# Kernel optimization log

Hardware: AMD Instinct MI355X
Metric: run time of the kernel (lower is better)

## Reference

```python
import math
import jax, jax.numpy as jnp
import numpy as np

B, S, D = 2, 2048, 512
H = 8
DH = D // H  # 64
FF = 2048


def _uniform(key, shape, c):
    return jax.random.uniform(key, shape, jnp.float32, -c, c)


def setup_inputs() -> dict:
    key = jax.random.key(0)
    ks = jax.random.split(key, 16)
    x = jax.random.normal(ks[0], (B, S, D), jnp.float32)
    c_qkv = math.sqrt(6 / (D + DH))
    wq = _uniform(ks[1], (H, D, DH), c_qkv)
    wk = _uniform(ks[2], (H, D, DH), c_qkv)
    wv = _uniform(ks[3], (H, D, DH), c_qkv)
    bq = jnp.zeros((H, DH), jnp.float32)
    bk = jnp.zeros((H, DH), jnp.float32)
    bv = jnp.zeros((H, DH), jnp.float32)
    c_o = math.sqrt(6 / (H * DH + D))
    wo = _uniform(ks[4], (H * DH, D), c_o)  # stored as (in, out)
    bo = jnp.zeros((D,), jnp.float32)
    gamma1 = jnp.ones((D,), jnp.float32)
    beta1 = jnp.zeros((D,), jnp.float32)
    c_ff = math.sqrt(6 / (D + FF))
    w1 = _uniform(ks[5], (D, FF), c_ff)
    b1 = jnp.zeros((FF,), jnp.float32)
    w2 = _uniform(ks[6], (FF, D), c_ff)
    b2 = jnp.zeros((D,), jnp.float32)
    gamma2 = jnp.ones((D,), jnp.float32)
    beta2 = jnp.zeros((D,), jnp.float32)
    return dict(x=x, wq=wq, bq=bq, wk=wk, bk=bk, wv=wv, bv=bv, wo=wo, bo=bo,
                gamma1=gamma1, beta1=beta1, w1=w1, b1=b1, w2=w2, b2=b2,
                gamma2=gamma2, beta2=beta2)


def _layernorm(x, gamma, beta):
    # matches torch: (x - mean) / std(unbiased=False), no epsilon in denom
    mean = jnp.mean(x, axis=-1, keepdims=True)
    var = jnp.mean((x - mean) ** 2, axis=-1, keepdims=True)
    return gamma * (x - mean) / jnp.sqrt(var) + beta


def reference(x, wq, bq, wk, bk, wv, bv, wo, bo, gamma1, beta1, w1, b1, w2, b2, gamma2, beta2):
    # multi-head attention: all heads batched in one einsum (same math as the per-head loop)
    q = jnp.einsum('bsd,hde->bhse', x, wq) + bq[None, :, None, :]
    k = jnp.einsum('bsd,hde->bhse', x, wk) + bk[None, :, None, :]
    v = jnp.einsum('bsd,hde->bhse', x, wv) + bv[None, :, None, :]
    scores = jnp.einsum('bhse,bhte->bhst', q, k) / math.sqrt(DH)  # [B,H,S,S]
    attn = jax.nn.softmax(scores, axis=-1)
    y = jnp.einsum('bhst,bhte->bhse', attn, v)  # [B,H,S,DH]
    y = y.transpose(0, 2, 1, 3).reshape(B, S, H * DH)
    y = y @ wo + bo
    # residual + LN (dropout is identity in eval)
    y = _layernorm(y + x, gamma1, beta1)
    # feedforward
    f = jax.nn.relu(y @ w1 + b1) @ w2 + b2
    out = _layernorm(f + y, gamma2, beta2)
    return out
```

## Files before the change

kernel.cpp:

```cpp
#include <hip/hip_runtime.h>

typedef __bf16 bf16;
typedef __attribute__((ext_vector_type(8))) __bf16 bf16x8;
typedef __attribute__((ext_vector_type(4))) float f32x4;
typedef __attribute__((ext_vector_type(16))) float f32x16;

#define DEV __device__ __forceinline__

DEV f32x4 mfma16(bf16x8 a, bf16x8 b, f32x4 c) {
  return __builtin_amdgcn_mfma_f32_16x16x32_bf16(a, b, c, 0, 0, 0);
}
DEV f32x16 mfma32(bf16x8 a, bf16x8 b, f32x16 c) {
  return __builtin_amdgcn_mfma_f32_32x32x16_bf16(a, b, c, 0, 0, 0);
}
DEV void gll16(const bf16* g, bf16* l) {
  __builtin_amdgcn_global_load_lds(
      (const __attribute__((address_space(1))) void*)g,
      (__attribute__((address_space(3))) void*)l, 16, 0, 0);
}
DEV unsigned cvtpk(float a, float b) {
  unsigned r;
  asm("v_cvt_pk_bf16_f32 %0, %1, %2" : "=v"(r) : "v"(a), "v"(b));
  return r;
}
DEV void pl32swap(unsigned& x, unsigned& y) {
  asm("v_permlane32_swap_b32 %0, %1" : "+v"(x), "+v"(y));
}

__global__ __launch_bounds__(256) void prep_k(
    const float* __restrict__ x, const float* __restrict__ wq,
    const float* __restrict__ wk, const float* __restrict__ wv,
    const float* __restrict__ wo, const float* __restrict__ w1,
    const float* __restrict__ w2, const float* __restrict__ bq,
    const float* __restrict__ bk, const float* __restrict__ bv,
    bf16* __restrict__ xb, bf16* __restrict__ wqkvT, bf16* __restrict__ woT,
    bf16* __restrict__ w1T, bf16* __restrict__ w2T, float* __restrict__ cb) {
  const int blk = blockIdx.x, tid = threadIdx.x;
  if (blk < 1024) {
    int i = blk * 256 + tid;
    const float4* p = (const float4*)x + (size_t)i * 2;
    float4 a = p[0], b = p[1];
    bf16x8 o;
    o[0] = (bf16)a.x; o[1] = (bf16)a.y; o[2] = (bf16)a.z; o[3] = (bf16)a.w;
    o[4] = (bf16)b.x; o[5] = (bf16)b.y; o[6] = (bf16)b.z; o[7] = (bf16)b.w;
    ((bf16x8*)xb)[i] = o;
    return;
  }
  if (blk == 1792) {
    for (int i = tid; i < 1536; i += 256)
      cb[i] = i < 512 ? bq[i] : (i < 1024 ? bk[i - 512] : bv[i - 1024]);
    return;
  }
  __shared__ float tile[64][65];
  const int t = blk - 1024;
  const float* src;
  bf16* dst;
  int C, Rout, r0, c0;
  if (t < 192) {
    int mat = t / 64, rem = t % 64, head = rem >> 3, rt = rem & 7;
    src = (mat == 0 ? wq : mat == 1 ? wk : wv) + head * 32768;
    dst = wqkvT + (size_t)(mat * 8 + head) * 32768;
    C = 64; Rout = 512; r0 = rt * 64; c0 = 0;
  } else if (t < 256) {
    int t2 = t - 192;
    src = wo; dst = woT; C = 512; Rout = 512;
    r0 = (t2 >> 3) * 64; c0 = (t2 & 7) * 64;
  } else if (t < 512) {
    int t2 = t - 256;
    src = w1; dst = w1T; C = 2048; Rout = 512;
    r0 = (t2 >> 5) * 64; c0 = (t2 & 31) * 64;
  } else {
    int t2 = t - 512;
    src = w2; dst = w2T; C = 512; Rout = 2048;
    r0 = (t2 >> 3) * 64; c0 = (t2 & 7) * 64;
  }
#pragma unroll
  for (int j = 0; j < 4; ++j) {
    int e = j * 256 + tid;
    int r = e >> 4, c4 = e & 15;
    float4 f = *(const float4*)(src + (size_t)(r0 + r) * C + c0 + c4 * 4);
    tile[r][c4 * 4 + 0] = f.x;
    tile[r][c4 * 4 + 1] = f.y;
    tile[r][c4 * 4 + 2] = f.z;
    tile[r][c4 * 4 + 3] = f.w;
  }
  __syncthreads();
  const int co = tid >> 2, rr0 = (tid & 3) * 16;
  bf16x8 o0, o1;
#pragma unroll
  for (int k = 0; k < 8; ++k) o0[k] = (bf16)tile[rr0 + k][co];
#pragma unroll
  for (int k = 0; k < 8; ++k) o1[k] = (bf16)tile[rr0 + 8 + k][co];
  bf16* dp = dst + (size_t)(c0 + co) * Rout + r0 + rr0;
  *(bf16x8*)dp = o0;
  *(bf16x8*)(dp + 8) = o1;
}

__global__ __launch_bounds__(256) void vtrans_k(const bf16* __restrict__ qkv,
                                                bf16* __restrict__ vtb) {
  __shared__ bf16 tile[64 * 68];
  const int tid = threadIdx.x;
  const int s0 = blockIdx.x * 64;
  const int bh = blockIdx.y, b = bh >> 3, hh = bh & 7;
  const bf16* src = qkv + 1024 + hh * 64;
#pragma unroll
  for (int j = 0; j < 2; ++j) {
    int slot = j * 256 + tid;
    int r = slot >> 3, cc = slot & 7;
    *(bf16x8*)(tile + r * 68 + cc * 8) =
        *(const bf16x8*)(src + (size_t)(b * 2048 + s0 + r) * 1536 + cc * 8);
  }
  __syncthreads();
  const int w = tid >> 6, lane = tid & 63;
#pragma unroll
  for (int sb2 = 0; sb2 < 2; ++sb2) {
    int sb = w * 2 + sb2;
    bf16x8 v;
#pragma unroll
    for (int jj = 0; jj < 8; ++jj) v[jj] = tile[(sb * 8 + jj) * 68 + lane];
    *(bf16x8*)(vtb + (size_t)bh * 131072 + (size_t)lane * 2048 + s0 + sb * 8) = v;
  }
}

template <int EPI>
__global__ __launch_bounds__(256) void gemmN64(
    const bf16* __restrict__ A, const bf16* __restrict__ Bt,
    const float* __restrict__ bias, float* __restrict__ outf,
    bf16* __restrict__ outb, int M, int N, int K, int klen) {
  __shared__ bf16 As[128 * 64];
  __shared__ bf16 Bs[64 * 64];
  const int tid = threadIdx.x;
  const int w = tid >> 6, l = tid & 63;
  const int lh = l & 15, lg = l >> 4;
  const int m0 = blockIdx.x * 128, n0 = blockIdx.y * 64;
  const int k0 = blockIdx.z * klen;
  const int mb = (w & 1) * 64, nb = (w >> 1) * 32;
  f32x4 acc[4][2] = {};
  for (int kt = k0; kt < k0 + klen; kt += 64) {
    __syncthreads();
#pragma unroll
    for (int j = 0; j < 4; ++j) {
      int slot = j * 256 + tid;
      int r = slot >> 3, cc = slot & 7;
      int kk = kt + ((cc ^ (r & 7)) << 3);
      gll16(A + (size_t)(m0 + r) * K + kk, As + slot * 8);
    }
#pragma unroll
    for (int j = 0; j < 2; ++j) {
      int slot = j * 256 + tid;
      int r = slot >> 3, cc = slot & 7;
      int kk = kt + ((cc ^ (r & 7)) << 3);
      gll16(Bt + (size_t)(n0 + r) * K + kk, Bs + slot * 8);
    }
    __syncthreads();
#pragma unroll
    for (int kk = 0; kk < 2; ++kk) {
      bf16x8 af[4], bfr[2];
#pragma unroll
      for (int mi = 0; mi < 4; ++mi) {
        int r = mb + mi * 16 + lh;
        af[mi] = *(const bf16x8*)(As + r * 64 + (((kk * 4 + lg) ^ (r & 7)) << 3));
      }
#pragma unroll
      for (int ni = 0; ni < 2; ++ni) {
        int r = nb + ni * 16 + lh;
        bfr[ni] = *(const bf16x8*)(Bs + r * 64 + (((kk * 4 + lg) ^ (r & 7)) << 3));
      }
#pragma unroll
      for (int mi = 0; mi < 4; ++mi)
#pragma unroll
        for (int ni = 0; ni < 2; ++ni)
          acc[mi][ni] = mfma16(af[mi], bfr[ni], acc[mi][ni]);
    }
  }
  float* op = (EPI == 0) ? outf + (size_t)blockIdx.z * M * N : nullptr;
#pragma unroll
  for (int mi = 0; mi < 4; ++mi)
#pragma unroll
    for (int ni = 0; ni < 2; ++ni)
#pragma unroll
      for (int i = 0; i < 4; ++i) {
        int row = m0 + mb + mi * 16 + lg * 4 + i;
        int col = n0 + nb + ni * 16 + lh;
        float v = acc[mi][ni][i];
        if (EPI == 0) {
          op[(size_t)row * N + col] = v;
        } else if (EPI == 1) {
          v += bias[col];
          outb[(size_t)row * N + col] = (bf16)fmaxf(v, 0.f);
        } else {
          v += bias[col];
          outb[(size_t)row * N + col] = (bf16)(col < 512 ? v * 0.125f : v);
        }
      }
}

__global__ __launch_bounds__(256) void attn_fwd5(
    const bf16* __restrict__ qkv,
    const bf16* __restrict__ vtb,
    bf16* __restrict__ Y) {
  __shared__ __align__(16) char lds[65536];
  const int tid = threadIdx.x;
  const int w = tid >> 6, lane = tid & 63;
  const int l31 = lane & 31, h = lane >> 5;
  const int bh = blockIdx.y, b = bh >> 3, hh = bh & 7;
  const int qt = blockIdx.x;
  const int wp = w & 1, half = w >> 1;
  const int q0 = qt * 64 + wp * 32;

  bf16x8 qf[4];
  {
    const size_t rowQ = (size_t)(b * 2048 + q0 + l31) * 1536 + hh * 64;
#pragma unroll
    for (int g = 0; g < 4; ++g)
      qf[g] = *(const bf16x8*)(qkv + rowQ + g * 16 + h * 8);
  }
  const bf16* Kp = qkv + 512 + hh * 64;
  const bf16* Vp = vtb + (size_t)bh * 131072;

  f32x16 oacc[2] = {};
  float m_run = -1e30f, l_run = 0.f;

#define KBUF(d, hf) ((bf16*)(lds + (d) * 32768 + (hf) * 16384))
#define VBUF(d, hf) ((bf16*)(lds + (d) * 32768 + (hf) * 16384 + 8192))

  auto stage = [&](int i, int d) {
#pragma unroll
    for (int hf = 0; hf < 2; ++hf) {
      const int k0 = hf * 1024 + i * 64;
#pragma unroll
      for (int j = 0; j < 2; ++j) {
        int slot = j * 256 + tid;
        int r = slot >> 3, cc = slot & 7;
        gll16(Kp + (size_t)(b * 2048 + k0 + r) * 1536 + ((cc ^ (r & 7)) << 3),
              KBUF(d, hf) + slot * 8);
        gll16(Vp + (size_t)r * 2048 + k0 + ((cc ^ (r & 7)) << 3),
              VBUF(d, hf) + slot * 8);
      }
    }
  };

  stage(0, 0);
  __syncthreads();
  for (int i = 0; i < 16; ++i) {
    const int d = i & 1;
    if (i < 15) stage(i + 1, d ^ 1);
    const bf16* Kt = KBUF(d, half);
    const bf16* Vt = VBUF(d, half);
    f32x16 st[2];
    __builtin_amdgcn_s_setprio(1);
#pragma unroll
    for (int kt = 0; kt < 2; ++kt) {
      f32x16 z = {};
      const int r = kt * 32 + l31;
#pragma unroll
      for (int g = 0; g < 4; ++g) {
        bf16x8 kf = *(const bf16x8*)(Kt + r * 64 + (((2 * g + h) ^ (r & 7)) << 3));
        z = mfma32(kf, qf[g], z);
      }
      st[kt] = z;
    }
    __builtin_amdgcn_s_setprio(0);
    float mx = -1e30f;
#pragma unroll
    for (int kt = 0; kt < 2; ++kt)
#pragma unroll
      for (int r = 0; r < 16; ++r) mx = fmaxf(mx, st[kt][r]);
    mx = fmaxf(mx, __shfl_xor(mx, 32, 64));
    const float m_new = fmaxf(m_run, mx);
    const float scl = __expf(m_run - m_new);
    m_run = m_new;
    float ps = 0.f;
#pragma unroll
    for (int kt = 0; kt < 2; ++kt)
#pragma unroll
      for (int r = 0; r < 16; ++r) {
        float e = __expf(st[kt][r] - m_new);
        st[kt][r] = e;
        ps += e;
      }
    ps += __shfl_xor(ps, 32, 64);
    l_run = l_run * scl + ps;
    oacc[0] = oacc[0] * scl;
    oacc[1] = oacc[1] * scl;
    bf16x8 pf[4];
#pragma unroll
    for (int kt = 0; kt < 2; ++kt)
#pragma unroll
      for (int g = 0; g < 2; ++g) {
        unsigned a0 = cvtpk(st[kt][8 * g + 0], st[kt][8 * g + 1]);
        unsigned a1 = cvtpk(st[kt][8 * g + 2], st[kt][8 * g + 3]);
        unsigned b0 = cvtpk(st[kt][8 * g + 4], st[kt][8 * g + 5]);
        unsigned b1 = cvtpk(st[kt][8 * g + 6], st[kt][8 * g + 7]);
        pl32swap(a0, b0);
        pl32swap(a1, b1);
        union { unsigned u[4]; bf16x8 v; } pk;
        pk.u[0] = a0; pk.u[1] = a1; pk.u[2] = b0; pk.u[3] = b1;
        pf[kt * 2 + g] = pk.v;
      }
    __builtin_amdgcn_s_setprio(1);
#pragma unroll
    for (int t = 0; t < 2; ++t) {
      const int r = t * 32 + l31;
#pragma unroll
      for (int kg = 0; kg < 4; ++kg) {
        bf16x8 vf = *(const bf16x8*)(Vt + r * 64 + (((2 * kg + h) ^ (r & 7)) << 3));
        oacc[t] = mfma32(vf, pf[kg], oacc[t]);
      }
    }
    __builtin_amdgcn_s_setprio(0);
    __syncthreads();
  }

  if (half == 1) {
    char* ob = lds + wp * 8192;
#pragma unroll
    for (int t = 0; t < 2; ++t)
#pragma unroll
      for (int c = 0; c < 4; ++c) {
        f32x4 v4 = {oacc[t][c * 4 + 0], oacc[t][c * 4 + 1],
                    oacc[t][c * 4 + 2], oacc[t][c * 4 + 3]};
        *(f32x4*)(ob + (t * 4 + c) * 1024 + lane * 16) = v4;
      }
    ((float2*)(lds + 32768))[wp * 64 + lane] = make_float2(m_run, l_run);
  }
  __syncthreads();
  bf16* Yt = (bf16*)(lds + 34816);
  if (half == 0) {
    float2 ml2 = ((const float2*)(lds + 32768))[wp * 64 + lane];
    const float mstar = fmaxf(m_run, ml2.x);
    const float e1 = __expf(m_run - mstar), e2 = __expf(ml2.x - mstar);
    const float lstar = l_run * e1 + ml2.y * e2;
    const float r1 = e1 / lstar, r2 = e2 / lstar;
    const char* ob = lds + wp * 8192;
#pragma unroll
    for (int t = 0; t < 2; ++t)
#pragma unroll
      for (int c = 0; c < 4; ++c) {
        f32x4 v4 = *(const f32x4*)(ob + (t * 4 + c) * 1024 + lane * 16);
#pragma unroll
        for (int j = 0; j < 4; ++j)
          oacc[t][c * 4 + j] = oacc[t][c * 4 + j] * r1 + v4[j] * r2;
      }
#pragma unroll
    for (int t = 0; t < 2; ++t)
#pragma unroll
      for (int r = 0; r < 16; ++r) {
        int dh = (r & 3) + 8 * (r >> 2) + 4 * h + 32 * t;
        Yt[(wp * 32 + l31) * 72 + dh] = (bf16)oacc[t][r];
      }
  }
  __syncthreads();
#pragma unroll
  for (int it = 0; it < 2; ++it) {
    int s = it * 256 + tid;
    int ql = s >> 3, cbk = s & 7;
    bf16x8 v = *(const bf16x8*)(Yt + ql * 72 + cbk * 8);
    *(bf16x8*)(Y + (size_t)(b * 2048 + qt * 64 + ql) * 512 + hh * 64 + cbk * 8) = v;
  }
#undef KBUF
#undef VBUF
}

__global__ __launch_bounds__(256) void add_ln1_k(
    const float* __restrict__ P,
    const float* __restrict__ xres, const float* __restrict__ bias,
    const float* __restrict__ gamma, const float* __restrict__ beta,
    bf16* __restrict__ outb) {
  const int row = blockIdx.x, tid = threadIdx.x;
  const size_t base = (size_t)row * 512;
  const float2 p0 = ((const float2*)(P + base))[tid];
  const float2 p1 = ((const float2*)(P + 2097152 + base))[tid];
  const float2 xr = ((const float2*)(xres + base))[tid];
  const int c = tid * 2;
  float s0 = p0.x + p1.x + bias[c] + xr.x;
  float s1 = p0.y + p1.y + bias[c + 1] + xr.y;
  float sum = s0 + s1;
#pragma unroll
  for (int m = 1; m < 64; m <<= 1) sum += __shfl_xor(sum, m, 64);
  __shared__ float part[4], part2[4];
  const int w = tid >> 6, l = tid & 63;
  if (l == 0) part[w] = sum;
  __syncthreads();
  const float mean = (part[0] + part[1] + part[2] + part[3]) * (1.f / 512.f);
  const float d0 = s0 - mean, d1 = s1 - mean;
  float vs = d0 * d0 + d1 * d1;
#pragma unroll
  for (int m = 1; m < 64; m <<= 1) vs += __shfl_xor(vs, m, 64);
  if (l == 0) part2[w] = vs;
  __syncthreads();
  const float var = (part2[0] + part2[1] + part2[2] + part2[3]) * (1.f / 512.f);
  const float inv = rsqrtf(var);
  outb[base + c] = (bf16)(gamma[c] * (d0 * inv) + beta[c]);
  outb[base + c + 1] = (bf16)(gamma[c + 1] * (d1 * inv) + beta[c + 1]);
}

__global__ __launch_bounds__(256) void add_ln2_k(
    const float* __restrict__ P,
    const bf16* __restrict__ rres, const float* __restrict__ bias,
    const float* __restrict__ gamma, const float* __restrict__ beta,
    float* __restrict__ outf) {
  const int row = blockIdx.x, tid = threadIdx.x;
  const size_t base = (size_t)row * 512;
  const float2 p0 = ((const float2*)(P + base))[tid];
  const float2 p1 = ((const float2*)(P + 2097152 + base))[tid];
  const int c = tid * 2;
  float s0 = p0.x + p1.x + bias[c] + (float)rres[base + c];
  float s1 = p0.y + p1.y + bias[c + 1] + (float)rres[base + c + 1];
  float sum = s0 + s1;
#pragma unroll
  for (int m = 1; m < 64; m <<= 1) sum += __shfl_xor(sum, m, 64);
  __shared__ float part[4], part2[4];
  const int w = tid >> 6, l = tid & 63;
  if (l == 0) part[w] = sum;
  __syncthreads();
  const float mean = (part[0] + part[1] + part[2] + part[3]) * (1.f / 512.f);
  const float d0 = s0 - mean, d1 = s1 - mean;
  float vs = d0 * d0 + d1 * d1;
#pragma unroll
  for (int m = 1; m < 64; m <<= 1) vs += __shfl_xor(vs, m, 64);
  if (l == 0) part2[w] = vs;
  __syncthreads();
  const float var = (part2[0] + part2[1] + part2[2] + part2[3]) * (1.f / 512.f);
  const float inv = rsqrtf(var);
  ((float2*)(outf + base))[tid] =
      make_float2(gamma[c] * (d0 * inv) + beta[c], gamma[c + 1] * (d1 * inv) + beta[c + 1]);
}

extern "C" void kernel_launch(void* const* d_in, const int* in_sizes, int n_in,
                              void* d_out, int out_size, void* d_ws, size_t ws_size,
                              hipStream_t stream) {
  const float* x = (const float*)d_in[0];
  const float* wq = (const float*)d_in[1];
  const float* bq = (const float*)d_in[2];
  const float* wk = (const float*)d_in[3];
  const float* bk = (const float*)d_in[4];
  const float* wv = (const float*)d_in[5];
  const float* bv = (const float*)d_in[6];
  const float* wo = (const float*)d_in[7];
  const float* bo = (const float*)d_in[8];
  const float* g1 = (const float*)d_in[9];
  const float* be1 = (const float*)d_in[10];
  const float* w1 = (const float*)d_in[11];
  const float* b1 = (const float*)d_in[12];
  const float* w2 = (const float*)d_in[13];
  const float* b2 = (const float*)d_in[14];
  const float* g2 = (const float*)d_in[15];
  const float* be2 = (const float*)d_in[16];

  char* ws = (char*)d_ws;
  bf16* xb    = (bf16*)(ws + 0);
  bf16* y1b   = (bf16*)(ws + 0);
  bf16* wqkvT = (bf16*)(ws + 4194304);
  bf16* woT   = (bf16*)(ws + 5767168);
  bf16* w1T   = (bf16*)(ws + 6291456);
  bf16* w2T   = (bf16*)(ws + 8388608);
  float* cb   = (float*)(ws + 10485760);
  bf16* qkvb  = (bf16*)(ws + 10493952);
  float* t0   = (float*)(ws + 10493952);
  bf16* f1    = (bf16*)(ws + 10493952);
  bf16* vtb   = (bf16*)(ws + 23078656);
  bf16* yb    = (bf16*)(ws + 27272960);
  float* f2   = (float*)(ws + 27272960);

  prep_k<<<1793, 256, 0, stream>>>(x, wq, wk, wv, wo, w1, w2, bq, bk, bv,
                                   xb, wqkvT, woT, w1T, w2T, cb);

  gemmN64<2><<<dim3(32, 24, 1), 256, 0, stream>>>(xb, wqkvT, cb, nullptr, qkvb,
                                                  4096, 1536, 512, 512);
  vtrans_k<<<dim3(32, 16), 256, 0, stream>>>(qkvb, vtb);
  attn_fwd5<<<dim3(32, 16), 256, 0, stream>>>(qkvb, vtb, yb);
  gemmN64<0><<<dim3(32, 8, 2), 256, 0, stream>>>(yb, woT, nullptr, t0, nullptr,
                                                 4096, 512, 512, 256);
  add_ln1_k<<<4096, 256, 0, stream>>>(t0, x, bo, g1, be1, y1b);
  gemmN64<1><<<dim3(32, 32, 1), 256, 0, stream>>>(y1b, w1T, b1, nullptr, f1,
                                                  4096, 2048, 512, 512);
  gemmN64<0><<<dim3(32, 8, 2), 256, 0, stream>>>(f1, w2T, nullptr, f2, nullptr,
                                                 4096, 512, 2048, 1024);
  add_ln2_k<<<4096, 256, 0, stream>>>(f2, y1b, b2, g2, be2, (float*)d_out);
}
```

Baseline: 119.9 us.

## Split attention KV range across four wave pairs with 512-thread blocks

The attention kernel now runs 8 waves per block instead of 4, splitting the 2048-key range into four quarters instead of two. Each iteration loads one tile per quarter, and four partial softmax states are merged at the end. Double buffering is dropped for a single-buffer load-then-sync loop. The row max and row sum reductions become tree reductions to shorten dependency chains. The aim is more waves to hide latency and more MFMA parallelism, at the cost of unoverlapped loads, an extra sync per iteration and a larger merge step.

```diff
diff --git a/kernel.cpp b/kernel.cpp
--- a/kernel.cpp
+++ b/kernel.cpp
@@ -195,7 +195,7 @@
       }
 }
 
-__global__ __launch_bounds__(256) void attn_fwd5(
+__global__ __launch_bounds__(512) void attn_fwd6(
     const bf16* __restrict__ qkv,
     const bf16* __restrict__ vtb,
     bf16* __restrict__ Y) {
@@ -205,7 +205,7 @@
   const int l31 = lane & 31, h = lane >> 5;
   const int bh = blockIdx.y, b = bh >> 3, hh = bh & 7;
   const int qt = blockIdx.x;
-  const int wp = w & 1, half = w >> 1;
+  const int wp = w & 1, hx = w >> 1;
   const int q0 = qt * 64 + wp * 32;
 
   bf16x8 qf[4];
@@ -221,32 +221,26 @@
   f32x16 oacc[2] = {};
   float m_run = -1e30f, l_run = 0.f;
 
-#define KBUF(d, hf) ((bf16*)(lds + (d) * 32768 + (hf) * 16384))
-#define VBUF(d, hf) ((bf16*)(lds + (d) * 32768 + (hf) * 16384 + 8192))
-
-  auto stage = [&](int i, int d) {
-#pragma unroll
-    for (int hf = 0; hf < 2; ++hf) {
-      const int k0 = hf * 1024 + i * 64;
-#pragma unroll
-      for (int j = 0; j < 2; ++j) {
-        int slot = j * 256 + tid;
-        int r = slot >> 3, cc = slot & 7;
-        gll16(Kp + (size_t)(b * 2048 + k0 + r) * 1536 + ((cc ^ (r & 7)) << 3),
-              KBUF(d, hf) + slot * 8);
-        gll16(Vp + (size_t)r * 2048 + k0 + ((cc ^ (r & 7)) << 3),
-              VBUF(d, hf) + slot * 8);
-      }
+#define KB6(q4) ((bf16*)(lds + (q4) * 16384))
+#define VB6(q4) ((bf16*)(lds + (q4) * 16384 + 8192))
+
+  auto stage = [&](int it) {
+    const int r = tid >> 3, cc = tid & 7;
+#pragma unroll
+    for (int q4 = 0; q4 < 4; ++q4) {
+      const int k0 = q4 * 512 + it * 64;
+      gll16(Kp + (size_t)(b * 2048 + k0 + r) * 1536 + ((cc ^ (r & 7)) << 3),
+            KB6(q4) + tid * 8);
+      gll16(Vp + (size_t)r * 2048 + k0 + ((cc ^ (r & 7)) << 3),
+            VB6(q4) + tid * 8);
     }
   };
 
-  stage(0, 0);
-  __syncthreads();
-  for (int i = 0; i < 16; ++i) {
-    const int d = i & 1;
-    if (i < 15) stage(i + 1, d ^ 1);
-    const bf16* Kt = KBUF(d, half);
-    const bf16* Vt = VBUF(d, half);
+  for (int i = 0; i < 8; ++i) {
+    stage(i);
+    __syncthreads();
+    const bf16* Kt = KB6(hx);
+    const bf16* Vt = VB6(hx);
     f32x16 st[2];
     __builtin_amdgcn_s_setprio(1);
 #pragma unroll
@@ -261,25 +255,29 @@
       st[kt] = z;
     }
     __builtin_amdgcn_s_setprio(0);
-    float mx = -1e30f;
-#pragma unroll
-    for (int kt = 0; kt < 2; ++kt)
-#pragma unroll
-      for (int r = 0; r < 16; ++r) mx = fmaxf(mx, st[kt][r]);
-    mx = fmaxf(mx, __shfl_xor(mx, 32, 64));
+    float tm[16];
+#pragma unroll
+    for (int r = 0; r < 16; ++r) tm[r] = fmaxf(st[0][r], st[1][r]);
+#pragma unroll
+    for (int s = 8; s > 0; s >>= 1)
+#pragma unroll
+      for (int r = 0; r < s; ++r) tm[r] = fmaxf(tm[r], tm[r + s]);
+    float mx = fmaxf(tm[0], __shfl_xor(tm[0], 32, 64));
     const float m_new = fmaxf(m_run, mx);
     const float scl = __expf(m_run - m_new);
     m_run = m_new;
-    float ps = 0.f;
 #pragma unroll
     for (int kt = 0; kt < 2; ++kt)
 #pragma unroll
-      for (int r = 0; r < 16; ++r) {
-        float e = __expf(st[kt][r] - m_new);
-        st[kt][r] = e;
-        ps += e;
-      }
-    ps += __shfl_xor(ps, 32, 64);
+      for (int r = 0; r < 16; ++r) st[kt][r] = __expf(st[kt][r] - m_new);
+    float ts[16];
+#pragma unroll
+    for (int r = 0; r < 16; ++r) ts[r] = st[0][r] + st[1][r];
+#pragma unroll
+    for (int s = 8; s > 0; s >>= 1)
+#pragma unroll
+      for (int r = 0; r < s; ++r) ts[r] += ts[r + s];
+    float ps = ts[0] + __shfl_xor(ts[0], 32, 64);
     l_run = l_run * scl + ps;
     oacc[0] = oacc[0] * scl;
     oacc[1] = oacc[1] * scl;
@@ -312,8 +310,8 @@
     __syncthreads();
   }
 
-  if (half == 1) {
-    char* ob = lds + wp * 8192;
+  if (hx > 0) {
+    char* ob = lds + (hx - 1) * 16384 + wp * 8192;
 #pragma unroll
     for (int t = 0; t < 2; ++t)
 #pragma unroll
@@ -322,25 +320,43 @@
                     oacc[t][c * 4 + 2], oacc[t][c * 4 + 3]};
         *(f32x4*)(ob + (t * 4 + c) * 1024 + lane * 16) = v4;
       }
-    ((float2*)(lds + 32768))[wp * 64 + lane] = make_float2(m_run, l_run);
-  }
-  __syncthreads();
-  bf16* Yt = (bf16*)(lds + 34816);
-  if (half == 0) {
-    float2 ml2 = ((const float2*)(lds + 32768))[wp * 64 + lane];
-    const float mstar = fmaxf(m_run, ml2.x);
-    const float e1 = __expf(m_run - mstar), e2 = __expf(ml2.x - mstar);
-    const float lstar = l_run * e1 + ml2.y * e2;
-    const float r1 = e1 / lstar, r2 = e2 / lstar;
-    const char* ob = lds + wp * 8192;
+    if (h == 0)
+      ((float2*)(lds + 49152))[(hx * 2 + wp) * 32 + l31] = make_float2(m_run, l_run);
+  }
+  __syncthreads();
+  bf16* Yt = (bf16*)(lds + 51200);
+  if (hx == 0) {
+    float mj[3], lj[3];
+    float mstar = m_run;
+#pragma unroll
+    for (int j = 0; j < 3; ++j) {
+      float2 ml = ((const float2*)(lds + 49152))[((j + 1) * 2 + wp) * 32 + l31];
+      mj[j] = ml.x; lj[j] = ml.y;
+      mstar = fmaxf(mstar, mj[j]);
+    }
+    const float e0 = __expf(m_run - mstar);
+    float ej[3];
+    float lstar = l_run * e0;
+#pragma unroll
+    for (int j = 0; j < 3; ++j) { ej[j] = __expf(mj[j] - mstar); lstar += lj[j] * ej[j]; }
+    const float inv = 1.f / lstar;
+    const float r0 = e0 * inv;
 #pragma unroll
     for (int t = 0; t < 2; ++t)
 #pragma unroll
       for (int c = 0; c < 4; ++c) {
-        f32x4 v4 = *(const f32x4*)(ob + (t * 4 + c) * 1024 + lane * 16);
-#pragma unroll
-        for (int j = 0; j < 4; ++j)
-          oacc[t][c * 4 + j] = oacc[t][c * 4 + j] * r1 + v4[j] * r2;
+        f32x4 a4 = {oacc[t][c * 4 + 0] * r0, oacc[t][c * 4 + 1] * r0,
+                    oacc[t][c * 4 + 2] * r0, oacc[t][c * 4 + 3] * r0};
+#pragma unroll
+        for (int j = 0; j < 3; ++j) {
+          f32x4 v4 = *(const f32x4*)(lds + j * 16384 + wp * 8192 +
+                                     (t * 4 + c) * 1024 + lane * 16);
+          const float rj = ej[j] * inv;
+          a4[0] += v4[0] * rj; a4[1] += v4[1] * rj;
+          a4[2] += v4[2] * rj; a4[3] += v4[3] * rj;
+        }
+        oacc[t][c * 4 + 0] = a4[0]; oacc[t][c * 4 + 1] = a4[1];
+        oacc[t][c * 4 + 2] = a4[2]; oacc[t][c * 4 + 3] = a4[3];
       }
 #pragma unroll
     for (int t = 0; t < 2; ++t)
@@ -351,15 +367,13 @@
       }
   }
   __syncthreads();
-#pragma unroll
-  for (int it = 0; it < 2; ++it) {
-    int s = it * 256 + tid;
-    int ql = s >> 3, cbk = s & 7;
+  {
+    const int ql = tid >> 3, cbk = tid & 7;
     bf16x8 v = *(const bf16x8*)(Yt + ql * 72 + cbk * 8);
     *(bf16x8*)(Y + (size_t)(b * 2048 + qt * 64 + ql) * 512 + hh * 64 + cbk * 8) = v;
   }
-#undef KBUF
-#undef VBUF
+#undef KB6
+#undef VB6
 }
 
 __global__ __launch_bounds__(256) void add_ln1_k(
@@ -469,7 +483,7 @@
   gemmN64<2><<<dim3(32, 24, 1), 256, 0, stream>>>(xb, wqkvT, cb, nullptr, qkvb,
                                                   4096, 1536, 512, 512);
   vtrans_k<<<dim3(32, 16), 256, 0, stream>>>(qkvb, vtb);
-  attn_fwd5<<<dim3(32, 16), 256, 0, stream>>>(qkvb, vtb, yb);
+  attn_fwd6<<<dim3(32, 16), 512, 0, stream>>>(qkvb, vtb, yb);
   gemmN64<0><<<dim3(32, 8, 2), 256, 0, stream>>>(yb, woT, nullptr, t0, nullptr,
                                                  4096, 512, 512, 256);
   add_ln1_k<<<4096, 256, 0, stream>>>(t0, x, bo, g1, be1, y1b);
```

Measured after the change: 127.4 us. +6.2%, slower.
